# Kernel tuning notes

Hardware: AMD Instinct MI355X
Metric: run time of the kernel (lower is better)

The kernel has to match this reference:

```python
import jax, jax.numpy as jnp
import numpy as np

B, C, H, W = 8, 512, 64, 64
NH, D = 8, 64            # num_heads, head_dim (C = NH*D)
WH, WW = 8, 8            # window size
EPS = 1e-5
SCALE = D ** -0.5


def _layernorm(x, g, b):
    mu = jnp.mean(x, axis=-1, keepdims=True)
    var = jnp.mean((x - mu) ** 2, axis=-1, keepdims=True)
    return (x - mu) * jax.lax.rsqrt(var + EPS) * g + b


def _rope_cache(n, d):
    pos = jnp.arange(n, dtype=jnp.float32)
    inv_freq = 1.0 / (10000.0 ** (jnp.arange(0, d, 2, dtype=jnp.float32) / d))
    sinusoid = pos[:, None] * inv_freq[None, :]          # (n, d//2)
    return jnp.stack([jnp.sin(sinusoid), jnp.cos(sinusoid)], axis=-1).reshape(n, d)


def _apply_rope(x, rope):
    # x: (B, nH, N, d); rope: (N, d) packed [sin, cos] interleaved
    b, nh, n, d = x.shape
    x_ = x.reshape(b, nh, n, d // 2, 2)
    r = rope.reshape(n, d // 2, 2)
    sin, cos = r[..., 0], r[..., 1]                      # (N, d//2)
    x0, x1 = x_[..., 0], x_[..., 1]
    xr0 = x0 * cos - x1 * sin
    xr1 = x0 * sin + x1 * cos
    return jnp.stack([xr0, xr1], axis=-1).reshape(b, nh, n, d)


def _relative_index(wh, ww):
    ch, cw = np.meshgrid(np.arange(wh), np.arange(ww), indexing='ij')
    flat = np.stack([ch.reshape(-1), cw.reshape(-1)])    # (2, Ws)
    rel = flat[:, :, None] - flat[:, None, :]            # (2, Ws, Ws)
    rel = rel.transpose(1, 2, 0).astype(np.int64)
    rel[..., 0] += wh - 1
    rel[..., 1] += ww - 1
    rel[..., 0] *= 2 * ww - 1
    return jnp.asarray(rel.sum(-1))                      # (Ws, Ws)


def setup_inputs() -> dict:
    key = jax.random.key(0)
    ks = jax.random.split(key, 12)
    s = 0.02
    table_size = (2 * WH - 1) * (2 * WW - 1)
    return {
        'q':  jax.random.normal(ks[0], (B, C, H, W), jnp.float32),
        'kv': jax.random.normal(ks[1], (B, C, H, W), jnp.float32),
        'g_q':  jnp.ones((C,), jnp.float32),  'b_q_ln':  jnp.zeros((C,), jnp.float32),
        'g_kv': jnp.ones((C,), jnp.float32),  'b_kv_ln': jnp.zeros((C,), jnp.float32),
        'Wq': jax.random.normal(ks[2], (C, C), jnp.float32) * s, 'bq': jnp.zeros((C,), jnp.float32),
        'Wk': jax.random.normal(ks[3], (C, C), jnp.float32) * s, 'bk': jnp.zeros((C,), jnp.float32),
        'Wv': jax.random.normal(ks[4], (C, C), jnp.float32) * s, 'bv': jnp.zeros((C,), jnp.float32),
        'Wo': jax.random.normal(ks[5], (C, C), jnp.float32) * s, 'bo': jnp.zeros((C,), jnp.float32),
        'bias_table': jax.random.normal(ks[6], (table_size, NH), jnp.float32) * s,
    }


def reference(q, kv, g_q, b_q_ln, g_kv, b_kv_ln, Wq, bq, Wk, bk, Wv, bv, Wo, bo, bias_table):
    N = H * W
    Hn, Wn = H // WH, W // WW
    nw = Hn * Wn
    Ws = WH * WW

    # flatten NCHW -> (B, N, C)
    q_seq = q.reshape(B, C, N).transpose(0, 2, 1)
    kv_seq = kv.reshape(B, C, N).transpose(0, 2, 1)
    q_seq = _layernorm(q_seq, g_q, b_q_ln)
    kv_seq = _layernorm(kv_seq, g_kv, b_kv_ln)

    Q = (q_seq @ Wq.T + bq).reshape(B, N, NH, D).transpose(0, 2, 1, 3)   # (B,nH,N,d)
    K = (kv_seq @ Wk.T + bk).reshape(B, N, NH, D).transpose(0, 2, 1, 3)
    V = (kv_seq @ Wv.T + bv).reshape(B, N, NH, D).transpose(0, 2, 1, 3)

    rope = _rope_cache(N, D)
    Q = _apply_rope(Q, rope)
    K = _apply_rope(K, rope)

    # window partition: (B,nH,H,W,d) -> (nH, B*nw, Ws, d); head-major to match torch cat order
    def part(x):
        x = x.reshape(B, NH, Hn, WH, Wn, WW, D)
        return x.transpose(1, 0, 2, 4, 3, 5, 6).reshape(NH, B * nw, Ws, D)

    Qw, Kw, Vw = part(Q), part(K), part(V)

    attn = jnp.einsum('hnqd,hnkd->hnqk', Qw, Kw) * SCALE                 # (nH, B*nw, Ws, Ws)
    rel_idx = _relative_index(WH, WW)
    bias = bias_table[rel_idx.reshape(-1)].reshape(Ws, Ws, NH).transpose(2, 0, 1)  # (nH, Ws, Ws)
    attn = attn + bias[:, None, :, :]
    attn = jax.nn.softmax(attn, axis=-1)
    out_w = jnp.einsum('hnqk,hnkd->hnqd', attn, Vw)                      # (nH, B*nw, Ws, d)

    # window reverse + head concat -> (B, N, C)
    out = out_w.reshape(NH, B, Hn, Wn, WH, WW, D)
    out = out.transpose(1, 2, 4, 3, 5, 0, 6).reshape(B, N, NH * D)

    out = out @ Wo.T + bo
    out = out + q_seq                                                    # residual w/ normed q (as in source)
    return out.transpose(0, 2, 1).reshape(B, C, H, W)
```

## Files before the change

kernel.cpp:

```cpp
#include <hip/hip_runtime.h>


typedef unsigned short u16;
typedef __bf16 bf16x8 __attribute__((ext_vector_type(8)));
typedef float f32x4 __attribute__((ext_vector_type(4)));
typedef u16 u16x8 __attribute__((ext_vector_type(8)));
typedef u16 u16x4 __attribute__((ext_vector_type(4)));

__device__ __forceinline__ u16 f2bf(float f) {
    __bf16 h = (__bf16)f;
    return __builtin_bit_cast(u16, h);
}
__device__ __forceinline__ float bf2f(u16 u) {
    return (float)__builtin_bit_cast(__bf16, u);
}
__device__ __forceinline__ f32x4 mfma16(bf16x8 a, bf16x8 b, f32x4 c) {
    return __builtin_amdgcn_mfma_f32_16x16x32_bf16(a, b, c, 0, 0, 0);
}
__device__ __forceinline__ void gl_lds16(const u16* g, u16* l) {
    __builtin_amdgcn_global_load_lds((const __attribute__((address_space(1))) void*)g,
                                     (__attribute__((address_space(3))) void*)l, 16, 0, 0);
}
__device__ __forceinline__ int swapb(int n) {
    return (n & 0xE07) | ((n & 0x1C0) >> 3) | ((n & 0x038) << 3);
}

__global__ __launch_bounds__(256) void setup_kernel(
    const float* __restrict__ Wq, const float* __restrict__ Wk,
    const float* __restrict__ Wv, const float* __restrict__ Wo,
    const float* __restrict__ btab,
    u16* __restrict__ wq, u16* __restrict__ wk,
    u16* __restrict__ wv, u16* __restrict__ wo,
    float* __restrict__ rope, float* __restrict__ biasf)
{
    int idx = blockIdx.x * 256 + threadIdx.x;
    {
        int w = idx >> 18, e = idx & 262143;
        const float* src = (w == 0) ? Wq : (w == 1) ? Wk : (w == 2) ? Wv : Wo;
        u16* dst = (w == 0) ? wq : (w == 1) ? wk : (w == 2) ? wv : wo;
        dst[e] = f2bf(src[e]);
    }
    if (idx < 131072) {
        int n = idx >> 5, j = idx & 31;
        float inv = powf(10000.0f, -(float)j / 32.0f);
        float a = (float)n * inv;
        float s, c;
        sincosf(a, &s, &c);
        rope[n * 64 + 2 * j] = s;
        rope[n * 64 + 2 * j + 1] = c;
    }
    if (idx < 32768) {
        int q = idx & 63, pp = (idx >> 6) & 63, h = idx >> 12;
        int r1 = pp >> 3, c1 = pp & 7, r2 = q >> 3, c2 = q & 7;
        int ri = (r1 - r2 + 7) * 15 + (c1 - c2 + 7);
        biasf[idx] = btab[ri * 8 + h];
    }
}

__global__ __launch_bounds__(256) void ln_kernel(
    const float* __restrict__ x, const float* __restrict__ g,
    const float* __restrict__ be, u16* __restrict__ out)
{
    __shared__ u16 sX[512 * 36];
    __shared__ float sS[1024];
    __shared__ float sQ[1024];
    __shared__ float sMu[32], sInv[32];

    const int tid = threadIdx.x;
    const int b = blockIdx.x >> 7, grp = blockIdx.x & 127;
    const int nbase = grp << 5;
    const int t4 = tid & 7;
    const int cg = tid >> 3;

    const float* xp = x + ((size_t)b << 21) + nbase + (t4 << 2);
    float sm[4] = {0.f, 0.f, 0.f, 0.f}, sq2[4] = {0.f, 0.f, 0.f, 0.f};
#pragma unroll 4
    for (int it = 0; it < 16; it++) {
        int c = (it << 5) + cg;
        f32x4 v = *(const f32x4*)&xp[(size_t)c << 12];
        u16x4 h;
#pragma unroll
        for (int r = 0; r < 4; r++) {
            sm[r] += v[r];
            sq2[r] += v[r] * v[r];
            h[r] = f2bf(v[r]);
        }
        *(u16x4*)&sX[c * 36 + (t4 << 2)] = h;
    }
#pragma unroll
    for (int r = 0; r < 4; r++) {
        sS[tid * 4 + r] = sm[r];
        sQ[tid * 4 + r] = sq2[r];
    }
    __syncthreads();
    if (tid < 32) {
        int t4v = tid >> 2, r = tid & 3;
        float a = 0.f, q2 = 0.f;
#pragma unroll
        for (int c2 = 0; c2 < 32; c2++) {
            int i2 = ((c2 << 3) + t4v) * 4 + r;
            a += sS[i2];
            q2 += sQ[i2];
        }
        float mu = a * (1.f / 512.f);
        float var = q2 * (1.f / 512.f) - mu * mu;
        sMu[tid] = mu;
        sInv[tid] = rsqrtf(var + 1e-5f);
    }
    __syncthreads();

    const int t = tid >> 3;
    const int cs = (tid & 7) << 3;
    float mu = sMu[t], inv = sInv[t];
    int p = swapb(nbase + t);
    size_t orow = ((size_t)((b << 12) + p)) * 512;
#pragma unroll
    for (int it = 0; it < 8; it++) {
        int c0 = cs + (it << 6);
        f32x4 g0 = *(const f32x4*)&g[c0];
        f32x4 g1 = *(const f32x4*)&g[c0 + 4];
        f32x4 e0 = *(const f32x4*)&be[c0];
        f32x4 e1 = *(const f32x4*)&be[c0 + 4];
        u16x8 o;
#pragma unroll
        for (int k = 0; k < 8; k++) {
            float v = bf2f(sX[(c0 + k) * 36 + t]);
            float gg = (k < 4) ? g0[k] : g1[k - 4];
            float bb = (k < 4) ? e0[k] : e1[k - 4];
            o[k] = f2bf((v - mu) * inv * gg + bb);
        }
        *(u16x8*)&out[orow + c0] = o;
    }
}

__global__ __launch_bounds__(512, 2) void gemm_qkv(
    const u16* __restrict__ qn, const u16* __restrict__ kvn,
    const u16* __restrict__ wq, const u16* __restrict__ wk, const u16* __restrict__ wv,
    const float* __restrict__ bq, const float* __restrict__ bk, const float* __restrict__ bv,
    const float* __restrict__ rope,
    u16* __restrict__ Qr, u16* __restrict__ Kr, u16* __restrict__ VT)
{
    __shared__ __align__(16) u16 smem[65536];

    const int bid = blockIdx.x;
    const int swz = (bid & 7) * 96 + (bid >> 3);
    const int kind = swz >> 8;
    const int rem = swz & 255;
    const int n0 = (rem >> 7) << 8;
    const int m0 = (rem & 127) << 8;

    const u16* Asrc = (kind == 0) ? qn : kvn;
    const u16* W = (kind == 0) ? wq : (kind == 1) ? wk : wv;
    const float* bias = (kind == 0) ? bq : (kind == 1) ? bk : bv;

    const int tid = threadIdx.x;
    const int lane = tid & 63, wid = tid >> 6;
    const int ln = lane & 15, lq = lane >> 4;
    const int wr = wid >> 2, wc = wid & 3;

    const int rr = tid >> 2;
    const int cc = (tid & 3) ^ ((tid >> 3) & 3);
    const u16* aSt = Asrc + (size_t)(m0 + rr) * 512 + cc * 8;
    const u16* bSt = W + (size_t)(n0 + rr) * 512 + cc * 8;

    const int AX = 0, BX = 16384, AY = 32768, BY = 49152;

#define SB() __builtin_amdgcn_sched_barrier(0)
#define BARRIER() do { SB(); __builtin_amdgcn_s_barrier(); SB(); } while (0)
#define VM4() asm volatile("s_waitcnt vmcnt(4)" ::: "memory")
#define VM0() asm volatile("s_waitcnt vmcnt(0)" ::: "memory")
#define STAGE_A(base, kt, kk) do { \
        const u16* _g = aSt + (kt) * 64 + (kk) * 32; \
        gl_lds16(_g, &smem[(base) + (kk) * 8192 + wid * 512]); \
        gl_lds16(_g + 65536, &smem[(base) + (kk) * 8192 + 4096 + wid * 512]); \
    } while (0)
#define STAGE_B(base, kt, kk) do { \
        const u16* _g = bSt + (kt) * 64 + (kk) * 32; \
        gl_lds16(_g, &smem[(base) + (kk) * 8192 + wid * 512]); \
        gl_lds16(_g + 65536, &smem[(base) + (kk) * 8192 + 4096 + wid * 512]); \
    } while (0)

    const int swzc = lq ^ ((ln >> 1) & 3);
    const int aOff = wr * 4096 + ln * 32 + swzc * 8;
    const int bOff = wc * 2048 + ln * 32 + swzc * 8;

#define LDA(base, kk, mh) do { \
        Af[0] = *(const bf16x8*)&smem[(base) + (kk) * 8192 + (mh) * 2048 + 0 * 512 + aOff]; \
        Af[1] = *(const bf16x8*)&smem[(base) + (kk) * 8192 + (mh) * 2048 + 1 * 512 + aOff]; \
        Af[2] = *(const bf16x8*)&smem[(base) + (kk) * 8192 + (mh) * 2048 + 2 * 512 + aOff]; \
        Af[3] = *(const bf16x8*)&smem[(base) + (kk) * 8192 + (mh) * 2048 + 3 * 512 + aOff]; \
    } while (0)
#define LDB(base, kk) do { \
        Bf[0] = *(const bf16x8*)&smem[(base) + (kk) * 8192 + 0 * 512 + bOff]; \
        Bf[1] = *(const bf16x8*)&smem[(base) + (kk) * 8192 + 1 * 512 + bOff]; \
        Bf[2] = *(const bf16x8*)&smem[(base) + (kk) * 8192 + 2 * 512 + bOff]; \
        Bf[3] = *(const bf16x8*)&smem[(base) + (kk) * 8192 + 3 * 512 + bOff]; \
    } while (0)
#define MMA(mh) do { \
        __builtin_amdgcn_s_setprio(1); \
        _Pragma("unroll") \
        for (int fi = 0; fi < 4; ++fi) \
            _Pragma("unroll") \
            for (int j = 0; j < 4; ++j) \
                acc[(mh) * 4 + fi][j] = mfma16(Af[fi], Bf[j], acc[(mh) * 4 + fi][j]); \
        __builtin_amdgcn_s_setprio(0); \
    } while (0)

    f32x4 acc[8][4] = {};

    STAGE_A(AX, 0, 0);
    STAGE_B(BX, 0, 0);
    STAGE_A(AX, 0, 1);
    STAGE_B(BX, 0, 1);
    VM4();
    BARRIER();

#pragma unroll
    for (int it = 0; it < 4; ++it) {
        const bool last = (it == 3);
        bf16x8 Af[4], Bf[4];
        LDA(AX, 0, 0);
        LDB(BX, 0);
        STAGE_A(AY, 2 * it + 1, 0);
        BARRIER();
        MMA(0);
        BARRIER();
        LDA(AX, 0, 1);
        STAGE_B(BY, 2 * it + 1, 0);
        BARRIER();
        MMA(1);
        VM4();
        BARRIER();
        LDA(AX, 1, 0);
        LDB(BX, 1);
        STAGE_A(AY, 2 * it + 1, 1);
        BARRIER();
        MMA(0);
        BARRIER();
        LDA(AX, 1, 1);
        STAGE_B(BY, 2 * it + 1, 1);
        BARRIER();
        MMA(1);
        VM4();
        BARRIER();
        LDA(AY, 0, 0);
        LDB(BY, 0);
        if (!last) STAGE_A(AX, 2 * it + 2, 0);
        BARRIER();
        MMA(0);
        BARRIER();
        LDA(AY, 0, 1);
        if (!last) STAGE_B(BX, 2 * it + 2, 0);
        BARRIER();
        MMA(1);
        if (!last) {
            VM4();
        } else {
            VM0();
        }
        BARRIER();
        LDA(AY, 1, 0);
        LDB(BY, 1);
        if (!last) STAGE_A(AX, 2 * it + 2, 1);
        BARRIER();
        MMA(0);
        BARRIER();
        LDA(AY, 1, 1);
        if (!last) STAGE_B(BX, 2 * it + 2, 1);
        BARRIER();
        MMA(1);
        if (!last) VM4();
        BARRIER();
    }

#undef SB
#undef BARRIER
#undef VM4
#undef VM0
#undef STAGE_A
#undef STAGE_B
#undef LDA
#undef LDB
#undef MMA

    float bj[4];
#pragma unroll
    for (int j = 0; j < 4; ++j) bj[j] = bias[n0 + wc * 64 + j * 16 + ln];

    u16* sU = smem;

    if (kind < 2) {
        u16* Out = (kind == 0) ? Qr : Kr;
#pragma unroll
        for (int g = 0; g < 4; ++g) {
            __syncthreads();
            if (wr == (g >> 1)) {
                const int i0 = (g & 1) * 4;
#pragma unroll
                for (int di = 0; di < 4; ++di)
#pragma unroll
                    for (int j = 0; j < 4; ++j)
#pragma unroll
                        for (int r = 0; r < 4; ++r)
                            sU[(di * 16 + lq * 4 + r) * 264 + wc * 64 + j * 16 + ln] =
                                f2bf(acc[i0 + di][j][r] + bj[j]);
            }
            __syncthreads();
#pragma unroll
            for (int it = 0; it < 4; ++it) {
                int idx = it * 512 + tid;
                int row = idx >> 5;
                int cseg = (idx & 31) << 3;
                u16x8 v = *(const u16x8*)&sU[row * 264 + cseg];
                int t = m0 + g * 64 + row;
                int n = swapb(t & 4095);
                float f[8];
#pragma unroll
                for (int k = 0; k < 8; k++) f[k] = bf2f(v[k]);
                {
                    int d0 = cseg & 63;
                    const float* rp = &rope[n * 64 + d0];
                    f32x4 r0 = *(const f32x4*)rp;
                    f32x4 r1 = *(const f32x4*)(rp + 4);
#pragma unroll
                    for (int pp = 0; pp < 4; pp++) {
                        float sn = (pp < 2) ? r0[2 * pp] : r1[2 * (pp - 2)];
                        float cs2 = (pp < 2) ? r0[2 * pp + 1] : r1[2 * (pp - 2) + 1];
                        float x0 = f[2 * pp], x1 = f[2 * pp + 1];
                        f[2 * pp] = x0 * cs2 - x1 * sn;
                        f[2 * pp + 1] = x0 * sn + x1 * cs2;
                    }
                }
                u16x8 o;
#pragma unroll
                for (int k = 0; k < 8; k++) o[k] = f2bf(f[k]);
                *(u16x8*)&Out[(size_t)t * 512 + n0 + cseg] = o;
            }
        }
    } else {
        const int wq0 = m0 & 4095;
        const int bb = m0 >> 12;
#pragma unroll
        for (int g = 0; g < 4; ++g) {
            __syncthreads();
            if (wc == g) {
#pragma unroll
                for (int i = 0; i < 8; ++i)
#pragma unroll
                    for (int j = 0; j < 4; ++j) {
                        u16x4 pk;
#pragma unroll
                        for (int r = 0; r < 4; ++r) pk[r] = f2bf(acc[i][j][r] + bj[j]);
                        *(u16x4*)&sU[(j * 16 + ln) * 264 + wr * 128 + i * 16 + lq * 4] = pk;
                    }
            }
            __syncthreads();
#pragma unroll
            for (int it = 0; it < 4; ++it) {
                int idx = it * 512 + tid;
                int col = idx >> 5;
                int ch = (idx & 31) << 3;
                u16x8 v = *(const u16x8*)&sU[col * 264 + ch];
                int c = n0 + g * 64 + col;
                int hh = c >> 6, dd = c & 63;
                *(u16x8*)&VT[((size_t)((((bb << 3) + hh) << 6) + dd)) * 4096 + wq0 + ch] = v;
            }
        }
    }
}

__global__ __launch_bounds__(256) void gemm_out(
    const u16* __restrict__ A, const u16* __restrict__ Bw,
    const float* __restrict__ bias, const u16* __restrict__ qn,
    float* __restrict__ Out)
{
    __shared__ u16 sA[128 * 32];
    __shared__ u16 sB[128 * 32];
    __shared__ u16 sR[128 * 136];

    const int m0 = blockIdx.x * 128;
    const int n0 = blockIdx.y * 128;
    const int tid = threadIdx.x;
    const int lane = tid & 63, wave = tid >> 6;
    const int ln = lane & 15, lq = lane >> 4;
    const int wm = wave & 1, wn = wave >> 1;

    const int srow = wave * 16 + (lane >> 2);
    const int sseg = (lane & 3) << 3;
    const u16* gA0 = A + (size_t)(m0 + srow) * 512 + sseg;
    const u16* gA1 = gA0 + (size_t)64 * 512;
    const u16* gB0 = Bw + (size_t)(n0 + srow) * 512 + sseg;
    const u16* gB1 = gB0 + (size_t)64 * 512;
    u16* lA0 = &sA[wave * 16 * 32];
    u16* lA1 = &sA[(64 + wave * 16) * 32];
    u16* lB0 = &sB[wave * 16 * 32];
    u16* lB1 = &sB[(64 + wave * 16) * 32];

    f32x4 acc[4][4] = {};

    for (int kt = 0; kt < 512; kt += 32) {
        gl_lds16(gA0 + kt, lA0);
        gl_lds16(gA1 + kt, lA1);
        gl_lds16(gB0 + kt, lB0);
        gl_lds16(gB1 + kt, lB1);
        __syncthreads();
        bf16x8 af[4], bfr[4];
#pragma unroll
        for (int i = 0; i < 4; i++)
            af[i] = *(const bf16x8*)&sA[(wm * 64 + i * 16 + ln) * 32 + lq * 8];
#pragma unroll
        for (int j = 0; j < 4; j++)
            bfr[j] = *(const bf16x8*)&sB[(wn * 64 + j * 16 + ln) * 32 + lq * 8];
#pragma unroll
        for (int i = 0; i < 4; i++)
#pragma unroll
            for (int j = 0; j < 4; j++)
                acc[i][j] = mfma16(af[i], bfr[j], acc[i][j]);
        __syncthreads();
    }

#pragma unroll
    for (int it = 0; it < 8; it++) {
        int idx = it * 256 + tid;
        int row = idx >> 4, c8 = (idx & 15) << 3;
        *(u16x8*)&sR[row * 136 + c8] = *(const u16x8*)&qn[(size_t)(m0 + row) * 512 + n0 + c8];
    }
    __syncthreads();

    int cj[4];
    float bj[4];
#pragma unroll
    for (int j = 0; j < 4; j++) {
        cj[j] = n0 + wn * 64 + j * 16 + ln;
        bj[j] = bias[cj[j]];
    }
#pragma unroll
    for (int i = 0; i < 4; i++) {
        int t0 = m0 + wm * 64 + i * 16 + lq * 4;
        int bb = t0 >> 12;
        int nb = swapb(t0 & 4095);
        int lrow = wm * 64 + i * 16 + lq * 4;
#pragma unroll
        for (int j = 0; j < 4; j++) {
            int lcol = wn * 64 + j * 16 + ln;
            f32x4 v;
#pragma unroll
            for (int r = 0; r < 4; r++)
                v[r] = acc[i][j][r] + bj[j] + bf2f(sR[(lrow + r) * 136 + lcol]);
            *(f32x4*)&Out[((size_t)((bb << 9) + cj[j]) << 12) + nb] = v;
        }
    }
}

__global__ __launch_bounds__(256) void attn_kernel(
    const u16* __restrict__ Q, const u16* __restrict__ K, const u16* __restrict__ VT,
    const float* __restrict__ biasf, u16* __restrict__ Out)
{
    __shared__ u16 sQ[64 * 72];
    __shared__ u16 sK[64 * 72];
    __shared__ u16 sVT[64 * 72];
    __shared__ u16 sP[4][16 * 72];

    const int tid = threadIdx.x;
    const int h = blockIdx.x & 7;
    const int w = (blockIdx.x >> 3) & 63;
    const int b = blockIdx.x >> 9;
    const int lane = tid & 63, wave = tid >> 6;
    const int ln = lane & 15, lq = lane >> 4;

    const size_t qrow0 = (size_t)(b << 12) + w * 64;
    const size_t vrow0 = ((size_t)(((b << 3) + h) << 6)) * 4096 + w * 64;

#pragma unroll
    for (int ii = 0; ii < 2; ii++) {
        int idx = ii * 256 + tid;
        int row = idx >> 3, ch = (idx & 7) << 3;
        size_t ga = (qrow0 + row) * 512 + h * 64 + ch;
        *(u16x8*)&sQ[row * 72 + ch] = *(const u16x8*)&Q[ga];
        *(u16x8*)&sK[row * 72 + ch] = *(const u16x8*)&K[ga];
        *(u16x8*)&sVT[row * 72 + ch] = *(const u16x8*)&VT[vrow0 + (size_t)row * 4096 + ch];
    }
    __syncthreads();

    f32x4 s[4] = {};
#pragma unroll
    for (int ks = 0; ks < 2; ks++) {
        bf16x8 a = *(const bf16x8*)&sQ[(wave * 16 + ln) * 72 + ks * 32 + lq * 8];
#pragma unroll
        for (int j = 0; j < 4; j++) {
            bf16x8 bb = *(const bf16x8*)&sK[(j * 16 + ln) * 72 + ks * 32 + lq * 8];
            s[j] = mfma16(a, bb, s[j]);
        }
    }

    float sv[4][4];
#pragma unroll
    for (int r = 0; r < 4; r++) {
        const float* bp = &biasf[((h * 64 + wave * 16 + lq * 4 + r) << 6) + ln];
#pragma unroll
        for (int j = 0; j < 4; j++) sv[r][j] = s[j][r] * 0.125f + bp[j * 16];
    }
#pragma unroll
    for (int r = 0; r < 4; r++) {
        float m = fmaxf(fmaxf(sv[r][0], sv[r][1]), fmaxf(sv[r][2], sv[r][3]));
        m = fmaxf(m, __shfl_xor(m, 1));
        m = fmaxf(m, __shfl_xor(m, 2));
        m = fmaxf(m, __shfl_xor(m, 4));
        m = fmaxf(m, __shfl_xor(m, 8));
        float sum = 0.f;
#pragma unroll
        for (int j = 0; j < 4; j++) {
            sv[r][j] = __expf(sv[r][j] - m);
            sum += sv[r][j];
        }
        sum += __shfl_xor(sum, 1);
        sum += __shfl_xor(sum, 2);
        sum += __shfl_xor(sum, 4);
        sum += __shfl_xor(sum, 8);
        float rinv = 1.f / sum;
#pragma unroll
        for (int j = 0; j < 4; j++)
            sP[wave][(lq * 4 + r) * 72 + j * 16 + ln] = f2bf(sv[r][j] * rinv);
    }

    f32x4 o[4] = {};
#pragma unroll
    for (int ks = 0; ks < 2; ks++) {
        bf16x8 a = *(const bf16x8*)&sP[wave][ln * 72 + ks * 32 + lq * 8];
#pragma unroll
        for (int jd = 0; jd < 4; jd++) {
            bf16x8 bb = *(const bf16x8*)&sVT[(jd * 16 + ln) * 72 + ks * 32 + lq * 8];
            o[jd] = mfma16(a, bb, o[jd]);
        }
    }

#pragma unroll
    for (int r = 0; r < 4; r++)
#pragma unroll
        for (int jd = 0; jd < 4; jd++)
            sQ[(wave * 16 + lq * 4 + r) * 72 + jd * 16 + ln] = f2bf(o[jd][r]);
    __syncthreads();
#pragma unroll
    for (int ii = 0; ii < 2; ii++) {
        int idx = ii * 256 + tid;
        int row = idx >> 3, ch = (idx & 7) << 3;
        *(u16x8*)&Out[(qrow0 + row) * 512 + h * 64 + ch] = *(const u16x8*)&sQ[row * 72 + ch];
    }
}

extern "C" void kernel_launch(void* const* d_in, const int* in_sizes, int n_in,
                              void* d_out, int out_size, void* d_ws, size_t ws_size,
                              hipStream_t stream)
{
    const float* q    = (const float*)d_in[0];
    const float* kv   = (const float*)d_in[1];
    const float* g_q  = (const float*)d_in[2];
    const float* b_q  = (const float*)d_in[3];
    const float* g_kv = (const float*)d_in[4];
    const float* b_kv = (const float*)d_in[5];
    const float* Wq   = (const float*)d_in[6];
    const float* bq   = (const float*)d_in[7];
    const float* Wk   = (const float*)d_in[8];
    const float* bk   = (const float*)d_in[9];
    const float* Wv   = (const float*)d_in[10];
    const float* bv   = (const float*)d_in[11];
    const float* Wo   = (const float*)d_in[12];
    const float* bo   = (const float*)d_in[13];
    const float* btab = (const float*)d_in[14];

    char* ws = (char*)d_ws;
    u16* qn      = (u16*)(ws);
    u16* kvn     = (u16*)(ws + 33554432);
    u16* VT      = (u16*)(ws + 67108864);
    float* rope  = (float*)(ws + 100663296);
    float* biasf = (float*)(ws + 101711872);
    u16* wq      = (u16*)(ws + 101842944);
    u16* wk      = (u16*)(ws + 102367232);
    u16* wv      = (u16*)(ws + 102891520);
    u16* wo      = (u16*)(ws + 103415808);
    u16* aout    = kvn;
    u16* Qr      = (u16*)d_out;
    u16* Kr      = Qr + 16777216;

    setup_kernel<<<4096, 256, 0, stream>>>(Wq, Wk, Wv, Wo, btab, wq, wk, wv, wo, rope, biasf);
    ln_kernel<<<1024, 256, 0, stream>>>(q, g_q, b_q, qn);
    ln_kernel<<<1024, 256, 0, stream>>>(kv, g_kv, b_kv, kvn);
    gemm_qkv<<<768, 512, 0, stream>>>(qn, kvn, wq, wk, wv, bq, bk, bv, rope, Qr, Kr, VT);
    attn_kernel<<<4096, 256, 0, stream>>>(Qr, Kr, VT, biasf, aout);
    gemm_out<<<dim3(256, 4), 256, 0, stream>>>(aout, wo, bo, qn, (float*)d_out);
}
```

Measured before the change: 350.6 us.

## Merge setup and layernorm kernels; use pipelined 256x256 GEMM for output projection

Folds the weight-conversion/rope/bias setup kernel and both layernorm launches into one prep kernel, dispatching work by block index, which removes two launches and lets the independent work overlap. Replaces the simple 128x128 single-buffered output GEMM with the same 8-phase double-buffered 256x256 pipeline used by the QKV GEMM, made reusable through a macro. The new output GEMM launches only 256 blocks of 512 threads, so it may underfill the GPU. It also stages the residual through LDS in four chunks.

```diff
diff --git a/kernel.cpp b/kernel.cpp
--- a/kernel.cpp
+++ b/kernel.cpp
@@ -25,49 +25,59 @@
     return (n & 0xE07) | ((n & 0x1C0) >> 3) | ((n & 0x038) << 3);
 }
 
-__global__ __launch_bounds__(256) void setup_kernel(
+__global__ __launch_bounds__(256) void prep_kernel(
+    const float* __restrict__ q, const float* __restrict__ kv,
+    const float* __restrict__ g_q, const float* __restrict__ b_q,
+    const float* __restrict__ g_kv, const float* __restrict__ b_kv,
     const float* __restrict__ Wq, const float* __restrict__ Wk,
     const float* __restrict__ Wv, const float* __restrict__ Wo,
     const float* __restrict__ btab,
+    u16* __restrict__ qn, u16* __restrict__ kvn,
     u16* __restrict__ wq, u16* __restrict__ wk,
     u16* __restrict__ wv, u16* __restrict__ wo,
     float* __restrict__ rope, float* __restrict__ biasf)
 {
-    int idx = blockIdx.x * 256 + threadIdx.x;
-    {
-        int w = idx >> 18, e = idx & 262143;
-        const float* src = (w == 0) ? Wq : (w == 1) ? Wk : (w == 2) ? Wv : Wo;
-        u16* dst = (w == 0) ? wq : (w == 1) ? wk : (w == 2) ? wv : wo;
-        dst[e] = f2bf(src[e]);
-    }
-    if (idx < 131072) {
-        int n = idx >> 5, j = idx & 31;
-        float inv = powf(10000.0f, -(float)j / 32.0f);
-        float a = (float)n * inv;
-        float s, c;
-        sincosf(a, &s, &c);
-        rope[n * 64 + 2 * j] = s;
-        rope[n * 64 + 2 * j + 1] = c;
-    }
-    if (idx < 32768) {
-        int q = idx & 63, pp = (idx >> 6) & 63, h = idx >> 12;
-        int r1 = pp >> 3, c1 = pp & 7, r2 = q >> 3, c2 = q & 7;
-        int ri = (r1 - r2 + 7) * 15 + (c1 - c2 + 7);
-        biasf[idx] = btab[ri * 8 + h];
-    }
-}
-
-__global__ __launch_bounds__(256) void ln_kernel(
-    const float* __restrict__ x, const float* __restrict__ g,
-    const float* __restrict__ be, u16* __restrict__ out)
-{
     __shared__ u16 sX[512 * 36];
     __shared__ float sS[1024];
-    __shared__ float sQ[1024];
+    __shared__ float sQm[1024];
     __shared__ float sMu[32], sInv[32];
 
+    const int bidx = blockIdx.x;
     const int tid = threadIdx.x;
-    const int b = blockIdx.x >> 7, grp = blockIdx.x & 127;
+
+    if (bidx >= 2048) {
+        int idx = (bidx - 2048) * 256 + tid;
+        {
+            int w = idx >> 18, e = idx & 262143;
+            const float* src = (w == 0) ? Wq : (w == 1) ? Wk : (w == 2) ? Wv : Wo;
+            u16* dst = (w == 0) ? wq : (w == 1) ? wk : (w == 2) ? wv : wo;
+            dst[e] = f2bf(src[e]);
+        }
+        if (idx < 131072) {
+            int n = idx >> 5, j = idx & 31;
+            float inv = powf(10000.0f, -(float)j / 32.0f);
+            float a = (float)n * inv;
+            float s, c;
+            sincosf(a, &s, &c);
+            rope[n * 64 + 2 * j] = s;
+            rope[n * 64 + 2 * j + 1] = c;
+        }
+        if (idx < 32768) {
+            int qq = idx & 63, pp = (idx >> 6) & 63, h = idx >> 12;
+            int r1 = pp >> 3, c1 = pp & 7, r2 = qq >> 3, c2 = qq & 7;
+            int ri = (r1 - r2 + 7) * 15 + (c1 - c2 + 7);
+            biasf[idx] = btab[ri * 8 + h];
+        }
+        return;
+    }
+
+    const float* x  = (bidx < 1024) ? q : kv;
+    const float* g  = (bidx < 1024) ? g_q : g_kv;
+    const float* be = (bidx < 1024) ? b_q : b_kv;
+    u16* out = (bidx < 1024) ? qn : kvn;
+    const int bid = bidx & 1023;
+
+    const int b = bid >> 7, grp = bid & 127;
     const int nbase = grp << 5;
     const int t4 = tid & 7;
     const int cg = tid >> 3;
@@ -90,7 +100,7 @@
 #pragma unroll
     for (int r = 0; r < 4; r++) {
         sS[tid * 4 + r] = sm[r];
-        sQ[tid * 4 + r] = sq2[r];
+        sQm[tid * 4 + r] = sq2[r];
     }
     __syncthreads();
     if (tid < 32) {
@@ -100,7 +110,7 @@
         for (int c2 = 0; c2 < 32; c2++) {
             int i2 = ((c2 << 3) + t4v) * 4 + r;
             a += sS[i2];
-            q2 += sQ[i2];
+            q2 += sQm[i2];
         }
         float mu = a * (1.f / 512.f);
         float var = q2 * (1.f / 512.f) - mu * mu;
@@ -132,38 +142,6 @@
         *(u16x8*)&out[orow + c0] = o;
     }
 }
-
-__global__ __launch_bounds__(512, 2) void gemm_qkv(
-    const u16* __restrict__ qn, const u16* __restrict__ kvn,
-    const u16* __restrict__ wq, const u16* __restrict__ wk, const u16* __restrict__ wv,
-    const float* __restrict__ bq, const float* __restrict__ bk, const float* __restrict__ bv,
-    const float* __restrict__ rope,
-    u16* __restrict__ Qr, u16* __restrict__ Kr, u16* __restrict__ VT)
-{
-    __shared__ __align__(16) u16 smem[65536];
-
-    const int bid = blockIdx.x;
-    const int swz = (bid & 7) * 96 + (bid >> 3);
-    const int kind = swz >> 8;
-    const int rem = swz & 255;
-    const int n0 = (rem >> 7) << 8;
-    const int m0 = (rem & 127) << 8;
-
-    const u16* Asrc = (kind == 0) ? qn : kvn;
-    const u16* W = (kind == 0) ? wq : (kind == 1) ? wk : wv;
-    const float* bias = (kind == 0) ? bq : (kind == 1) ? bk : bv;
-
-    const int tid = threadIdx.x;
-    const int lane = tid & 63, wid = tid >> 6;
-    const int ln = lane & 15, lq = lane >> 4;
-    const int wr = wid >> 2, wc = wid & 3;
-
-    const int rr = tid >> 2;
-    const int cc = (tid & 3) ^ ((tid >> 3) & 3);
-    const u16* aSt = Asrc + (size_t)(m0 + rr) * 512 + cc * 8;
-    const u16* bSt = W + (size_t)(n0 + rr) * 512 + cc * 8;
-
-    const int AX = 0, BX = 16384, AY = 32768, BY = 49152;
 
 #define SB() __builtin_amdgcn_sched_barrier(0)
 #define BARRIER() do { SB(); __builtin_amdgcn_s_barrier(); SB(); } while (0)
@@ -179,11 +157,6 @@
         gl_lds16(_g, &smem[(base) + (kk) * 8192 + wid * 512]); \
         gl_lds16(_g + 65536, &smem[(base) + (kk) * 8192 + 4096 + wid * 512]); \
     } while (0)
-
-    const int swzc = lq ^ ((ln >> 1) & 3);
-    const int aOff = wr * 4096 + ln * 32 + swzc * 8;
-    const int bOff = wc * 2048 + ln * 32 + swzc * 8;
-
 #define LDA(base, kk, mh) do { \
         Af[0] = *(const bf16x8*)&smem[(base) + (kk) * 8192 + (mh) * 2048 + 0 * 512 + aOff]; \
         Af[1] = *(const bf16x8*)&smem[(base) + (kk) * 8192 + (mh) * 2048 + 1 * 512 + aOff]; \
@@ -206,72 +179,230 @@
         __builtin_amdgcn_s_setprio(0); \
     } while (0)
 
+#define MAIN_LOOP_8PHASE() \
+    STAGE_A(AX, 0, 0); \
+    STAGE_B(BX, 0, 0); \
+    STAGE_A(AX, 0, 1); \
+    STAGE_B(BX, 0, 1); \
+    VM4(); \
+    BARRIER(); \
+    _Pragma("unroll") \
+    for (int it = 0; it < 4; ++it) { \
+        const bool last = (it == 3); \
+        bf16x8 Af[4], Bf[4]; \
+        LDA(AX, 0, 0); LDB(BX, 0); STAGE_A(AY, 2 * it + 1, 0); \
+        BARRIER(); MMA(0); BARRIER(); \
+        LDA(AX, 0, 1); STAGE_B(BY, 2 * it + 1, 0); \
+        BARRIER(); MMA(1); VM4(); BARRIER(); \
+        LDA(AX, 1, 0); LDB(BX, 1); STAGE_A(AY, 2 * it + 1, 1); \
+        BARRIER(); MMA(0); BARRIER(); \
+        LDA(AX, 1, 1); STAGE_B(BY, 2 * it + 1, 1); \
+        BARRIER(); MMA(1); VM4(); BARRIER(); \
+        LDA(AY, 0, 0); LDB(BY, 0); if (!last) STAGE_A(AX, 2 * it + 2, 0); \
+        BARRIER(); MMA(0); BARRIER(); \
+        LDA(AY, 0, 1); if (!last) STAGE_B(BX, 2 * it + 2, 0); \
+        BARRIER(); MMA(1); \
+        if (!last) { VM4(); } else { VM0(); } \
+        BARRIER(); \
+        LDA(AY, 1, 0); LDB(BY, 1); if (!last) STAGE_A(AX, 2 * it + 2, 1); \
+        BARRIER(); MMA(0); BARRIER(); \
+        LDA(AY, 1, 1); if (!last) STAGE_B(BX, 2 * it + 2, 1); \
+        BARRIER(); MMA(1); if (!last) VM4(); BARRIER(); \
+    }
+
+__global__ __launch_bounds__(512, 2) void gemm_qkv(
+    const u16* __restrict__ qn, const u16* __restrict__ kvn,
+    const u16* __restrict__ wq, const u16* __restrict__ wk, const u16* __restrict__ wv,
+    const float* __restrict__ bq, const float* __restrict__ bk, const float* __restrict__ bv,
+    const float* __restrict__ rope,
+    u16* __restrict__ Qr, u16* __restrict__ Kr, u16* __restrict__ VT)
+{
+    __shared__ __align__(16) u16 smem[65536];
+
+    const int bid = blockIdx.x;
+    const int swz = (bid & 7) * 96 + (bid >> 3);
+    const int kind = swz >> 8;
+    const int rem = swz & 255;
+    const int n0 = (rem >> 7) << 8;
+    const int m0 = (rem & 127) << 8;
+
+    const u16* Asrc = (kind == 0) ? qn : kvn;
+    const u16* W = (kind == 0) ? wq : (kind == 1) ? wk : wv;
+    const float* bias = (kind == 0) ? bq : (kind == 1) ? bk : bv;
+
+    const int tid = threadIdx.x;
+    const int lane = tid & 63, wid = tid >> 6;
+    const int ln = lane & 15, lq = lane >> 4;
+    const int wr = wid >> 2, wc = wid & 3;
+
+    const int rr = tid >> 2;
+    const int cc = (tid & 3) ^ ((tid >> 3) & 3);
+    const u16* aSt = Asrc + (size_t)(m0 + rr) * 512 + cc * 8;
+    const u16* bSt = W + (size_t)(n0 + rr) * 512 + cc * 8;
+
+    const int AX = 0, BX = 16384, AY = 32768, BY = 49152;
+    const int swzc = lq ^ ((ln >> 1) & 3);
+    const int aOff = wr * 4096 + ln * 32 + swzc * 8;
+    const int bOff = wc * 2048 + ln * 32 + swzc * 8;
+
     f32x4 acc[8][4] = {};
 
-    STAGE_A(AX, 0, 0);
-    STAGE_B(BX, 0, 0);
-    STAGE_A(AX, 0, 1);
-    STAGE_B(BX, 0, 1);
-    VM4();
-    BARRIER();
-
-#pragma unroll
-    for (int it = 0; it < 4; ++it) {
-        const bool last = (it == 3);
-        bf16x8 Af[4], Bf[4];
-        LDA(AX, 0, 0);
-        LDB(BX, 0);
-        STAGE_A(AY, 2 * it + 1, 0);
-        BARRIER();
-        MMA(0);
-        BARRIER();
-        LDA(AX, 0, 1);
-        STAGE_B(BY, 2 * it + 1, 0);
-        BARRIER();
-        MMA(1);
-        VM4();
-        BARRIER();
-        LDA(AX, 1, 0);
-        LDB(BX, 1);
-        STAGE_A(AY, 2 * it + 1, 1);
-        BARRIER();
-        MMA(0);
-        BARRIER();
-        LDA(AX, 1, 1);
-        STAGE_B(BY, 2 * it + 1, 1);
-        BARRIER();
-        MMA(1);
-        VM4();
-        BARRIER();
-        LDA(AY, 0, 0);
-        LDB(BY, 0);
-        if (!last) STAGE_A(AX, 2 * it + 2, 0);
-        BARRIER();
-        MMA(0);
-        BARRIER();
-        LDA(AY, 0, 1);
-        if (!last) STAGE_B(BX, 2 * it + 2, 0);
-        BARRIER();
-        MMA(1);
-        if (!last) {
-            VM4();
-        } else {
-            VM0();
-        }
-        BARRIER();
-        LDA(AY, 1, 0);
-        LDB(BY, 1);
-        if (!last) STAGE_A(AX, 2 * it + 2, 1);
-        BARRIER();
-        MMA(0);
-        BARRIER();
-        LDA(AY, 1, 1);
-        if (!last) STAGE_B(BX, 2 * it + 2, 1);
-        BARRIER();
-        MMA(1);
-        if (!last) VM4();
-        BARRIER();
-    }
+    MAIN_LOOP_8PHASE();
+
+    float bj[4];
+#pragma unroll
+    for (int j = 0; j < 4; ++j) bj[j] = bias[n0 + wc * 64 + j * 16 + ln];
+
+    u16* sU = smem;
+
+    if (kind < 2) {
+        u16* Out = (kind == 0) ? Qr : Kr;
+#pragma unroll
+        for (int g = 0; g < 4; ++g) {
+            __syncthreads();
+            if (wr == (g >> 1)) {
+                const int i0 = (g & 1) * 4;
+#pragma unroll
+                for (int di = 0; di < 4; ++di)
+#pragma unroll
+                    for (int j = 0; j < 4; ++j)
+#pragma unroll
+                        for (int r = 0; r < 4; ++r)
+                            sU[(di * 16 + lq * 4 + r) * 264 + wc * 64 + j * 16 + ln] =
+                                f2bf(acc[i0 + di][j][r] + bj[j]);
+            }
+            __syncthreads();
+#pragma unroll
+            for (int it = 0; it < 4; ++it) {
+                int idx = it * 512 + tid;
+                int row = idx >> 5;
+                int cseg = (idx & 31) << 3;
+                u16x8 v = *(const u16x8*)&sU[row * 264 + cseg];
+                int t = m0 + g * 64 + row;
+                int n = swapb(t & 4095);
+                float f[8];
+#pragma unroll
+                for (int k = 0; k < 8; k++) f[k] = bf2f(v[k]);
+                {
+                    int d0 = cseg & 63;
+                    const float* rp = &rope[n * 64 + d0];
+                    f32x4 r0 = *(const f32x4*)rp;
+                    f32x4 r1 = *(const f32x4*)(rp + 4);
+#pragma unroll
+                    for (int pp = 0; pp < 4; pp++) {
+                        float sn = (pp < 2) ? r0[2 * pp] : r1[2 * (pp - 2)];
+                        float cs2 = (pp < 2) ? r0[2 * pp + 1] : r1[2 * (pp - 2) + 1];
+                        float x0 = f[2 * pp], x1 = f[2 * pp + 1];
+                        f[2 * pp] = x0 * cs2 - x1 * sn;
+                        f[2 * pp + 1] = x0 * sn + x1 * cs2;
+                    }
+                }
+                u16x8 o;
+#pragma unroll
+                for (int k = 0; k < 8; k++) o[k] = f2bf(f[k]);
+                *(u16x8*)&Out[(size_t)t * 512 + n0 + cseg] = o;
+            }
+        }
+    } else {
+        const int wq0 = m0 & 4095;
+        const int bb = m0 >> 12;
+#pragma unroll
+        for (int g = 0; g < 4; ++g) {
+            __syncthreads();
+            if (wc == g) {
+#pragma unroll
+                for (int i = 0; i < 8; ++i)
+#pragma unroll
+                    for (int j = 0; j < 4; ++j) {
+                        u16x4 pk;
+#pragma unroll
+                        for (int r = 0; r < 4; ++r) pk[r] = f2bf(acc[i][j][r] + bj[j]);
+                        *(u16x4*)&sU[(j * 16 + ln) * 264 + wr * 128 + i * 16 + lq * 4] = pk;
+                    }
+            }
+            __syncthreads();
+#pragma unroll
+            for (int it = 0; it < 4; ++it) {
+                int idx = it * 512 + tid;
+                int col = idx >> 5;
+                int ch = (idx & 31) << 3;
+                u16x8 v = *(const u16x8*)&sU[col * 264 + ch];
+                int c = n0 + g * 64 + col;
+                int hh = c >> 6, dd = c & 63;
+                *(u16x8*)&VT[((size_t)((((bb << 3) + hh) << 6) + dd)) * 4096 + wq0 + ch] = v;
+            }
+        }
+    }
+}
+
+__global__ __launch_bounds__(512, 2) void gemm_out(
+    const u16* __restrict__ A, const u16* __restrict__ Bw,
+    const float* __restrict__ bias, const u16* __restrict__ qn,
+    float* __restrict__ Out)
+{
+    __shared__ __align__(16) u16 smem[65536];
+
+    const int bid = blockIdx.x;
+    const int swz = (bid & 7) * 32 + (bid >> 3);
+    const int n0 = (swz >> 7) << 8;
+    const int m0 = (swz & 127) << 8;
+
+    const int tid = threadIdx.x;
+    const int lane = tid & 63, wid = tid >> 6;
+    const int ln = lane & 15, lq = lane >> 4;
+    const int wr = wid >> 2, wc = wid & 3;
+
+    const int rr = tid >> 2;
+    const int cc = (tid & 3) ^ ((tid >> 3) & 3);
+    const u16* aSt = A + (size_t)(m0 + rr) * 512 + cc * 8;
+    const u16* bSt = Bw + (size_t)(n0 + rr) * 512 + cc * 8;
+
+    const int AX = 0, BX = 16384, AY = 32768, BY = 49152;
+    const int swzc = lq ^ ((ln >> 1) & 3);
+    const int aOff = wr * 4096 + ln * 32 + swzc * 8;
+    const int bOff = wc * 2048 + ln * 32 + swzc * 8;
+
+    f32x4 acc[8][4] = {};
+
+    MAIN_LOOP_8PHASE();
+
+    float bj[4];
+#pragma unroll
+    for (int j = 0; j < 4; ++j) bj[j] = bias[n0 + wc * 64 + j * 16 + ln];
+
+    u16* sR = smem;
+#pragma unroll
+    for (int g = 0; g < 4; ++g) {
+        __syncthreads();
+#pragma unroll
+        for (int it = 0; it < 4; ++it) {
+            int idx = it * 512 + tid;
+            int row = idx >> 5, c8 = (idx & 31) << 3;
+            *(u16x8*)&sR[row * 264 + c8] =
+                *(const u16x8*)&qn[(size_t)(m0 + g * 64 + row) * 512 + n0 + c8];
+        }
+        __syncthreads();
+        if (wr == (g >> 1)) {
+            const int i0 = (g & 1) * 4;
+#pragma unroll
+            for (int di = 0; di < 4; ++di) {
+                int t0 = m0 + g * 64 + di * 16 + lq * 4;
+                int bb = t0 >> 12;
+                int nb = swapb(t0 & 4095);
+                int lr = di * 16 + lq * 4;
+#pragma unroll
+                for (int j = 0; j < 4; ++j) {
+                    int c = wc * 64 + j * 16 + ln;
+                    f32x4 v;
+#pragma unroll
+                    for (int r = 0; r < 4; ++r)
+                        v[r] = acc[i0 + di][j][r] + bj[j] + bf2f(sR[(lr + r) * 264 + c]);
+                    *(f32x4*)&Out[((size_t)((bb << 9) + n0 + c) << 12) + nb] = v;
+                }
+            }
+        }
+    }
+}
 
 #undef SB
 #undef BARRIER
@@ -282,175 +413,7 @@
 #undef LDA
 #undef LDB
 #undef MMA
-
-    float bj[4];
-#pragma unroll
-    for (int j = 0; j < 4; ++j) bj[j] = bias[n0 + wc * 64 + j * 16 + ln];
-
-    u16* sU = smem;
-
-    if (kind < 2) {
-        u16* Out = (kind == 0) ? Qr : Kr;
-#pragma unroll
-        for (int g = 0; g < 4; ++g) {
-            __syncthreads();
-            if (wr == (g >> 1)) {
-                const int i0 = (g & 1) * 4;
-#pragma unroll
-                for (int di = 0; di < 4; ++di)
-#pragma unroll
-                    for (int j = 0; j < 4; ++j)
-#pragma unroll
-                        for (int r = 0; r < 4; ++r)
-                            sU[(di * 16 + lq * 4 + r) * 264 + wc * 64 + j * 16 + ln] =
-                                f2bf(acc[i0 + di][j][r] + bj[j]);
-            }
-            __syncthreads();
-#pragma unroll
-            for (int it = 0; it < 4; ++it) {
-                int idx = it * 512 + tid;
-                int row = idx >> 5;
-                int cseg = (idx & 31) << 3;
-                u16x8 v = *(const u16x8*)&sU[row * 264 + cseg];
-                int t = m0 + g * 64 + row;
-                int n = swapb(t & 4095);
-                float f[8];
-#pragma unroll
-                for (int k = 0; k < 8; k++) f[k] = bf2f(v[k]);
-                {
-                    int d0 = cseg & 63;
-                    const float* rp = &rope[n * 64 + d0];
-                    f32x4 r0 = *(const f32x4*)rp;
-                    f32x4 r1 = *(const f32x4*)(rp + 4);
-#pragma unroll
-                    for (int pp = 0; pp < 4; pp++) {
-                        float sn = (pp < 2) ? r0[2 * pp] : r1[2 * (pp - 2)];
-                        float cs2 = (pp < 2) ? r0[2 * pp + 1] : r1[2 * (pp - 2) + 1];
-                        float x0 = f[2 * pp], x1 = f[2 * pp + 1];
-                        f[2 * pp] = x0 * cs2 - x1 * sn;
-                        f[2 * pp + 1] = x0 * sn + x1 * cs2;
-                    }
-                }
-                u16x8 o;
-#pragma unroll
-                for (int k = 0; k < 8; k++) o[k] = f2bf(f[k]);
-                *(u16x8*)&Out[(size_t)t * 512 + n0 + cseg] = o;
-            }
-        }
-    } else {
-        const int wq0 = m0 & 4095;
-        const int bb = m0 >> 12;
-#pragma unroll
-        for (int g = 0; g < 4; ++g) {
-            __syncthreads();
-            if (wc == g) {
-#pragma unroll
-                for (int i = 0; i < 8; ++i)
-#pragma unroll
-                    for (int j = 0; j < 4; ++j) {
-                        u16x4 pk;
-#pragma unroll
-                        for (int r = 0; r < 4; ++r) pk[r] = f2bf(acc[i][j][r] + bj[j]);
-                        *(u16x4*)&sU[(j * 16 + ln) * 264 + wr * 128 + i * 16 + lq * 4] = pk;
-                    }
-            }
-            __syncthreads();
-#pragma unroll
-            for (int it = 0; it < 4; ++it) {
-                int idx = it * 512 + tid;
-                int col = idx >> 5;
-                int ch = (idx & 31) << 3;
-                u16x8 v = *(const u16x8*)&sU[col * 264 + ch];
-                int c = n0 + g * 64 + col;
-                int hh = c >> 6, dd = c & 63;
-                *(u16x8*)&VT[((size_t)((((bb << 3) + hh) << 6) + dd)) * 4096 + wq0 + ch] = v;
-            }
-        }
-    }
-}
-
-__global__ __launch_bounds__(256) void gemm_out(
-    const u16* __restrict__ A, const u16* __restrict__ Bw,
-    const float* __restrict__ bias, const u16* __restrict__ qn,
-    float* __restrict__ Out)
-{
-    __shared__ u16 sA[128 * 32];
-    __shared__ u16 sB[128 * 32];
-    __shared__ u16 sR[128 * 136];
-
-    const int m0 = blockIdx.x * 128;
-    const int n0 = blockIdx.y * 128;
-    const int tid = threadIdx.x;
-    const int lane = tid & 63, wave = tid >> 6;
-    const int ln = lane & 15, lq = lane >> 4;
-    const int wm = wave & 1, wn = wave >> 1;
-
-    const int srow = wave * 16 + (lane >> 2);
-    const int sseg = (lane & 3) << 3;
-    const u16* gA0 = A + (size_t)(m0 + srow) * 512 + sseg;
-    const u16* gA1 = gA0 + (size_t)64 * 512;
-    const u16* gB0 = Bw + (size_t)(n0 + srow) * 512 + sseg;
-    const u16* gB1 = gB0 + (size_t)64 * 512;
-    u16* lA0 = &sA[wave * 16 * 32];
-    u16* lA1 = &sA[(64 + wave * 16) * 32];
-    u16* lB0 = &sB[wave * 16 * 32];
-    u16* lB1 = &sB[(64 + wave * 16) * 32];
-
-    f32x4 acc[4][4] = {};
-
-    for (int kt = 0; kt < 512; kt += 32) {
-        gl_lds16(gA0 + kt, lA0);
-        gl_lds16(gA1 + kt, lA1);
-        gl_lds16(gB0 + kt, lB0);
-        gl_lds16(gB1 + kt, lB1);
-        __syncthreads();
-        bf16x8 af[4], bfr[4];
-#pragma unroll
-        for (int i = 0; i < 4; i++)
-            af[i] = *(const bf16x8*)&sA[(wm * 64 + i * 16 + ln) * 32 + lq * 8];
-#pragma unroll
-        for (int j = 0; j < 4; j++)
-            bfr[j] = *(const bf16x8*)&sB[(wn * 64 + j * 16 + ln) * 32 + lq * 8];
-#pragma unroll
-        for (int i = 0; i < 4; i++)
-#pragma unroll
-            for (int j = 0; j < 4; j++)
-                acc[i][j] = mfma16(af[i], bfr[j], acc[i][j]);
-        __syncthreads();
-    }
-
-#pragma unroll
-    for (int it = 0; it < 8; it++) {
-        int idx = it * 256 + tid;
-        int row = idx >> 4, c8 = (idx & 15) << 3;
-        *(u16x8*)&sR[row * 136 + c8] = *(const u16x8*)&qn[(size_t)(m0 + row) * 512 + n0 + c8];
-    }
-    __syncthreads();
-
-    int cj[4];
-    float bj[4];
-#pragma unroll
-    for (int j = 0; j < 4; j++) {
-        cj[j] = n0 + wn * 64 + j * 16 + ln;
-        bj[j] = bias[cj[j]];
-    }
-#pragma unroll
-    for (int i = 0; i < 4; i++) {
-        int t0 = m0 + wm * 64 + i * 16 + lq * 4;
-        int bb = t0 >> 12;
-        int nb = swapb(t0 & 4095);
-        int lrow = wm * 64 + i * 16 + lq * 4;
-#pragma unroll
-        for (int j = 0; j < 4; j++) {
-            int lcol = wn * 64 + j * 16 + ln;
-            f32x4 v;
-#pragma unroll
-            for (int r = 0; r < 4; r++)
-                v[r] = acc[i][j][r] + bj[j] + bf2f(sR[(lrow + r) * 136 + lcol]);
-            *(f32x4*)&Out[((size_t)((bb << 9) + cj[j]) << 12) + nb] = v;
-        }
-    }
-}
+#undef MAIN_LOOP_8PHASE
 
 __global__ __launch_bounds__(256) void attn_kernel(
     const u16* __restrict__ Q, const u16* __restrict__ K, const u16* __restrict__ VT,
@@ -582,10 +545,10 @@
     u16* Qr      = (u16*)d_out;
     u16* Kr      = Qr + 16777216;
 
-    setup_kernel<<<4096, 256, 0, stream>>>(Wq, Wk, Wv, Wo, btab, wq, wk, wv, wo, rope, biasf);
-    ln_kernel<<<1024, 256, 0, stream>>>(q, g_q, b_q, qn);
-    ln_kernel<<<1024, 256, 0, stream>>>(kv, g_kv, b_kv, kvn);
+    prep_kernel<<<6144, 256, 0, stream>>>(q, kv, g_q, b_q, g_kv, b_kv,
+                                          Wq, Wk, Wv, Wo, btab,
+                                          qn, kvn, wq, wk, wv, wo, rope, biasf);
     gemm_qkv<<<768, 512, 0, stream>>>(qn, kvn, wq, wk, wv, bq, bk, bv, rope, Qr, Kr, VT);
     attn_kernel<<<4096, 256, 0, stream>>>(Qr, Kr, VT, biasf, aout);
-    gemm_out<<<dim3(256, 4), 256, 0, stream>>>(aout, wo, bo, qn, (float*)d_out);
-}
+    gemm_out<<<256, 512, 0, stream>>>(aout, wo, bo, qn, (float*)d_out);
+}
```

Result: no change. 344.2 us (-1.8%).
